# Optimization experiments

Hardware: AMD Instinct MI355X
Metric: run time of the kernel (lower is better)

## Reference

```python
import jax, jax.numpy as jnp
import numpy as np

VOXEL = 64          # voxel_size
MAX_DEPTH = 10.0    # depth_range[1]
SMIN, SMAX = -2.0, 2.0  # spatial_range


def setup_inputs() -> dict:
    key = jax.random.key(0)
    B, H, W = 32, 512, 512
    rgbd = jax.random.uniform(key, (B, 4, H, W), dtype=jnp.float32)
    # scale depth channel to a realistic metric range [0, 8) so that a
    # meaningful fraction of back-projected points falls inside [-2, 2]
    rgbd = rgbd.at[:, 3].multiply(8.0)
    return {"rgbd": rgbd}


def reference(rgbd):
    B, C, H, W = rgbd.shape
    V = VOXEL
    dt = rgbd.dtype

    rgb = jnp.transpose(rgbd[:, :3], (0, 2, 3, 1))   # [B,H,W,3]
    d = rgbd[:, 3]                                   # [B,H,W]

    # intrinsics is None -> default pinhole
    fx = fy = min(H, W) / 2.0
    cx, cy = W / 2.0, H / 2.0

    u = jnp.arange(W, dtype=dt)[None, None, :]       # column index (x)
    v = jnp.arange(H, dtype=dt)[None, :, None]       # row index (y)

    # depth -> pointcloud (per pixel)
    x = (u - cx) * d / fx
    y = (v - cy) * d / fy
    pts = jnp.stack([x, y, d], axis=-1)              # [B,H,W,3]

    depth_valid = (d > 0) & (d < MAX_DEPTH) & jnp.isfinite(d)

    # pointcloud -> voxel coordinates
    coords = jnp.round((pts - SMIN) / (SMAX - SMIN) * (V - 1)).astype(jnp.int32)
    in_range = jnp.all((coords >= 0) & (coords < V), axis=-1)
    mask = depth_valid & in_range                    # [B,H,W]
    coords = jnp.clip(coords, 0, V - 1)

    b_idx = jnp.arange(B, dtype=jnp.int32)[:, None, None]
    lin = ((b_idx * V + coords[..., 0]) * V + coords[..., 1]) * V + coords[..., 2]
    lin = lin.reshape(-1)                            # [B*H*W]
    w = mask.astype(dt).reshape(-1)                  # [B*H*W]

    nseg = B * V * V * V
    count = jax.ops.segment_sum(w, lin, num_segments=nseg)                 # [B*V^3]
    csum = jax.ops.segment_sum(rgb.reshape(-1, 3) * w[:, None], lin,
                               num_segments=nseg)                          # [B*V^3,3]

    occ = (count > 0).astype(dt)                                           # occupancy = 1 where any point lands
    color = jnp.where(count[:, None] > 0,
                      csum / jnp.maximum(count, 1.0)[:, None],
                      jnp.zeros((), dt))                                   # mean color per occupied voxel

    occ = occ.reshape(B, V, V, V)
    color = color.reshape(B, V, V, V, 3).transpose(0, 4, 1, 2, 3)
    return jnp.concatenate([occ[:, None], color], axis=1)  # [B,4,V,V,V]
```

## Files before the change

### kernel.cpp

```cpp
#include <hip/hip_runtime.h>
#include <math.h>


constexpr int V = 64;
constexpr int V3 = V * V * V;
constexpr int Wd = 512, Hd = 512;
constexpr int NPIX = Wd * Hd;
constexpr int NBUCKET = 32 * 64;
constexpr unsigned CAP = 30000;
constexpr float CQ = 32768.0f;

__device__ __forceinline__ bool unproject(int w, int h, float d,
                                          int& ix, int& iy, int& iz) {
    if (!(d > 0.0f) || !(d < 10.0f) || !isfinite(d)) return false;
    const float fx = 256.0f, cx = 256.0f, cy = 256.0f;
    float x = (((float)w - cx) * d) / fx;
    float y = (((float)h - cy) * d) / fx;
    float tx = rintf(((x + 2.0f) * 0.25f) * 63.0f);
    float ty = rintf(((y + 2.0f) * 0.25f) * 63.0f);
    float tz = rintf(((d + 2.0f) * 0.25f) * 63.0f);
    ix = (int)tx; iy = (int)ty; iz = (int)tz;
    return !(ix < 0 || ix >= V || iy < 0 || iy >= V ||
             iz < 0 || iz >= V);
}

__global__ void dtv_cursor_init(unsigned* __restrict__ cursor) {
    int i = blockIdx.x * blockDim.x + threadIdx.x;
    cursor[i] = (unsigned)i * CAP;
}

__global__ void __launch_bounds__(256)
dtv_append2(const float* __restrict__ rgbd,
            unsigned* __restrict__ cursor,
            unsigned long long* __restrict__ entries) {
    int blk = blockIdx.x;
    int b = blk >> 6, chunk = blk & 63, t = threadIdx.x;
    __shared__ unsigned lcnt[64];
    __shared__ unsigned labs[64];
    if (t < 64) lcnt[t] = 0;
    __syncthreads();

    const float* bb = rgbd + (size_t)b * 4 * NPIX;
    const float4* r4 = (const float4*)(bb) + chunk * 1024;
    const float4* g4 = (const float4*)(bb + (size_t)NPIX) + chunk * 1024;
    const float4* b4 = (const float4*)(bb + (size_t)2 * NPIX) + chunk * 1024;
    const float4* d4 = (const float4*)(bb + (size_t)3 * NPIX) + chunk * 1024;
    int pbase = chunk * 4096;

    unsigned meta[16];
#pragma unroll
    for (int i = 0; i < 4; ++i) {
        float4 dv = d4[t + i * 256];
        int p0 = pbase + 4 * (t + i * 256);
#pragma unroll
        for (int j = 0; j < 4; ++j) {
            float d = (j == 0) ? dv.x : (j == 1) ? dv.y : (j == 2) ? dv.z : dv.w;
            int pix = p0 + j;
            int h = pix >> 9, w = pix & (Wd - 1);
            int ix, iy, iz;
            if (unproject(w, h, d, ix, iy, iz)) {
                unsigned off = atomicAdd(&lcnt[ix], 1u);
                meta[i * 4 + j] = ((unsigned)ix << 24) | ((unsigned)iy << 18) |
                                  ((unsigned)iz << 12) | off;
            } else {
                meta[i * 4 + j] = 0xFFFFFFFFu;
            }
        }
    }
    __syncthreads();
    if (t < 64)
        labs[t] = lcnt[t] ? atomicAdd(&cursor[b * 64 + t], lcnt[t]) : 0u;
    __syncthreads();

#pragma unroll
    for (int i = 0; i < 4; ++i) {
        float4 rv = r4[t + i * 256];
        float4 gv = g4[t + i * 256];
        float4 bv = b4[t + i * 256];
#pragma unroll
        for (int j = 0; j < 4; ++j) {
            unsigned m = meta[i * 4 + j];
            if (m == 0xFFFFFFFFu) continue;
            unsigned ix = m >> 24, iy = (m >> 18) & 63u, iz = (m >> 12) & 63u;
            unsigned off = m & 0xFFFu;
            float r  = (j == 0) ? rv.x : (j == 1) ? rv.y : (j == 2) ? rv.z : rv.w;
            float g  = (j == 0) ? gv.x : (j == 1) ? gv.y : (j == 2) ? gv.z : gv.w;
            float bl = (j == 0) ? bv.x : (j == 1) ? bv.y : (j == 2) ? bv.z : bv.w;
            unsigned pos = labs[ix] + off;
            unsigned kk = (unsigned)(b * 64) + ix;
            if (pos >= (kk + 1) * CAP) continue;
            unsigned long long r16 = (unsigned long long)(unsigned)rintf(r  * CQ);
            unsigned long long g16 = (unsigned long long)(unsigned)rintf(g  * CQ);
            unsigned long long b16 = (unsigned long long)(unsigned)rintf(bl * CQ);
            entries[(size_t)pos] = ((unsigned long long)iy << 54) |
                                   ((unsigned long long)iz << 48) |
                                   (r16 << 32) | (g16 << 16) | b16;
        }
    }
}

__global__ void __launch_bounds__(256)
dtv_reduce2(const unsigned long long* __restrict__ entries,
            const unsigned* __restrict__ cursor,
            float* __restrict__ out) {
    int kk = blockIdx.x;
    int b = kk >> 6, ix = kk & 63, t = threadIdx.x;

    __shared__ unsigned long long ldsA[4096];
    __shared__ unsigned long long ldsB[4096];
#pragma unroll
    for (int i = 0; i < 16; ++i) {
        ldsA[t + i * 256] = 0ULL;
        ldsB[t + i * 256] = 0ULL;
    }
    __syncthreads();

    unsigned basew = (unsigned)kk * CAP;
    unsigned cnt = cursor[kk] - basew;
    if (cnt > CAP) cnt = CAP;
    for (unsigned e = t; e < cnt; e += 256) {
        unsigned long long p = entries[(size_t)basew + e];
        unsigned iy = (unsigned)(p >> 54) & 63u;
        unsigned iz = (unsigned)(p >> 48) & 63u;
        unsigned long long r16 = (p >> 32) & 0xFFFFULL;
        unsigned long long gb  = p & 0xFFFFFFFFULL;
        unsigned v = iy * 64u + iz;
        atomicAdd(&ldsA[v], (1ULL << 32) | r16);
        atomicAdd(&ldsB[v], ((gb >> 16) << 32) | (gb & 0xFFFFULL));
    }
    __syncthreads();

    float* p0 = out + (size_t)b * 4 * V3 + (size_t)ix * 4096;
#pragma unroll
    for (int i = 0; i < 16; ++i) {
        int v = t + i * 256;
        unsigned long long A = ldsA[v], Bw = ldsB[v];
        unsigned c = (unsigned)(A >> 32);
        float occ = 0.0f, r = 0.0f, g = 0.0f, bl = 0.0f;
        if (c) {
            float inv = 1.0f / (CQ * (float)c);
            occ = 1.0f;
            r  = (float)(unsigned)(A  & 0xFFFFFFFFULL) * inv;
            g  = (float)(unsigned)(Bw >> 32)            * inv;
            bl = (float)(unsigned)(Bw & 0xFFFFFFFFULL)  * inv;
        }
        p0[v]                  = occ;
        p0[(size_t)V3 + v]     = r;
        p0[(size_t)2 * V3 + v] = g;
        p0[(size_t)3 * V3 + v] = bl;
    }
}

__global__ void dtv_scatter_f32(const float* __restrict__ rgbd,
                                float* __restrict__ acc) {
    int idx = blockIdx.x * blockDim.x + threadIdx.x;
    int b   = idx >> 18;
    int pix = idx & (NPIX - 1);
    int h   = pix >> 9;
    int w   = pix & (Wd - 1);
    const float* base = rgbd + (size_t)b * 4 * NPIX;
    float d = base[(size_t)3 * NPIX + pix];
    int ix, iy, iz;
    if (!unproject(w, h, d, ix, iy, iz)) return;
    float r  = base[pix];
    float g  = base[(size_t)NPIX + pix];
    float bl = base[(size_t)2 * NPIX + pix];
    float* ob = acc + (size_t)b * 4 * V3;
    int vlin = (ix * V + iy) * V + iz;
    atomicAdd(ob + vlin, 1.0f);
    atomicAdd(ob + (size_t)V3 + vlin, r);
    atomicAdd(ob + (size_t)2 * V3 + vlin, g);
    atomicAdd(ob + (size_t)3 * V3 + vlin, bl);
}

__global__ void dtv_finalize_f32(float* __restrict__ out) {
    int idx = blockIdx.x * blockDim.x + threadIdx.x;
    int b    = idx >> 18;
    int vlin = idx & (V3 - 1);
    float* p = out + (size_t)b * 4 * V3;
    float c  = p[vlin];
    float r  = p[(size_t)V3 + vlin];
    float g  = p[(size_t)2 * V3 + vlin];
    float bl = p[(size_t)3 * V3 + vlin];
    bool occ = (c > 0.0f);
    p[vlin]                  = occ ? 1.0f : 0.0f;
    p[(size_t)V3 + vlin]     = occ ? (r / c)  : 0.0f;
    p[(size_t)2 * V3 + vlin] = occ ? (g / c)  : 0.0f;
    p[(size_t)3 * V3 + vlin] = occ ? (bl / c) : 0.0f;
}

extern "C" void kernel_launch(void* const* d_in, const int* in_sizes, int n_in,
                              void* d_out, int out_size, void* d_ws, size_t ws_size,
                              hipStream_t stream) {
    const float* rgbd = (const float*)d_in[0];
    float* out = (float*)d_out;
    const int B = in_sizes[0] / (4 * NPIX);

    size_t need = 8192 + (size_t)NBUCKET * CAP * sizeof(unsigned long long);

    if (B == 32 && ws_size >= need) {
        unsigned* cursor = (unsigned*)d_ws;
        unsigned long long* entries =
            (unsigned long long*)((char*)d_ws + 8192);
        dtv_cursor_init<<<NBUCKET / 256, 256, 0, stream>>>(cursor);
        dtv_append2    <<<2048, 256, 0, stream>>>(rgbd, cursor, entries);
        dtv_reduce2    <<<2048, 256, 0, stream>>>(entries, cursor, out);
    } else {
        hipMemsetAsync(d_out, 0, (size_t)out_size * sizeof(float), stream);
        int total_pix = B * NPIX;
        int total_vox = B * V3;
        dtv_scatter_f32 <<<(total_pix + 255) / 256, 256, 0, stream>>>(rgbd, out);
        dtv_finalize_f32<<<(total_vox + 255) / 256, 256, 0, stream>>>(out);
    }
}
```

Baseline: 286.7 us.

## Stage bucketed entries in LDS and write them out coalesced per bucket

The append kernel now halves the pixels per block (2048) and doubles the block count. Each block does a wave-level prefix scan over its 64 per-ix bucket counts, sorts its entries into shared memory by bucket, and then writes them to global memory in contiguous runs. Before, each thread scattered its 8-byte writes straight to global. The aim is to turn scattered global stores into mostly coalesced ones. The cost is an extra LDS pass, another barrier and about 20KB of shared memory per block, plus twice as many global cursor atomics.

```diff
diff --git a/kernel.cpp b/kernel.cpp
--- a/kernel.cpp
+++ b/kernel.cpp
@@ -9,6 +9,8 @@
 constexpr int NBUCKET = 32 * 64;
 constexpr unsigned CAP = 30000;
 constexpr float CQ = 32768.0f;
+constexpr int PPB = 2048;
+constexpr int CHUNKS = NPIX / PPB;
 
 __device__ __forceinline__ bool unproject(int w, int h, float d,
                                           int& ix, int& iy, int& iz) {
@@ -30,26 +32,31 @@
 }
 
 __global__ void __launch_bounds__(256)
-dtv_append2(const float* __restrict__ rgbd,
+dtv_append3(const float* __restrict__ rgbd,
             unsigned* __restrict__ cursor,
             unsigned long long* __restrict__ entries) {
     int blk = blockIdx.x;
-    int b = blk >> 6, chunk = blk & 63, t = threadIdx.x;
+    int b = blk >> 7, chunk = blk & (CHUNKS - 1), t = threadIdx.x;
+
     __shared__ unsigned lcnt[64];
+    __shared__ unsigned lpre[64];
     __shared__ unsigned labs[64];
+    __shared__ unsigned long long stage[PPB];
+    __shared__ unsigned short bkt[PPB];
+
     if (t < 64) lcnt[t] = 0;
     __syncthreads();
 
     const float* bb = rgbd + (size_t)b * 4 * NPIX;
-    const float4* r4 = (const float4*)(bb) + chunk * 1024;
-    const float4* g4 = (const float4*)(bb + (size_t)NPIX) + chunk * 1024;
-    const float4* b4 = (const float4*)(bb + (size_t)2 * NPIX) + chunk * 1024;
-    const float4* d4 = (const float4*)(bb + (size_t)3 * NPIX) + chunk * 1024;
-    int pbase = chunk * 4096;
-
-    unsigned meta[16];
-#pragma unroll
-    for (int i = 0; i < 4; ++i) {
+    const float4* r4 = (const float4*)(bb) + chunk * (PPB / 4);
+    const float4* g4 = (const float4*)(bb + (size_t)NPIX) + chunk * (PPB / 4);
+    const float4* b4 = (const float4*)(bb + (size_t)2 * NPIX) + chunk * (PPB / 4);
+    const float4* d4 = (const float4*)(bb + (size_t)3 * NPIX) + chunk * (PPB / 4);
+    int pbase = chunk * PPB;
+
+    unsigned meta[8];
+#pragma unroll
+    for (int i = 0; i < 2; ++i) {
         float4 dv = d4[t + i * 256];
         int p0 = pbase + 4 * (t + i * 256);
 #pragma unroll
@@ -68,12 +75,22 @@
         }
     }
     __syncthreads();
-    if (t < 64)
-        labs[t] = lcnt[t] ? atomicAdd(&cursor[b * 64 + t], lcnt[t]) : 0u;
-    __syncthreads();
-
-#pragma unroll
-    for (int i = 0; i < 4; ++i) {
+
+    if (t < 64) {
+        unsigned c = lcnt[t];
+        unsigned s = c;
+#pragma unroll
+        for (int off = 1; off < 64; off <<= 1) {
+            unsigned v = __shfl_up(s, off, 64);
+            if (t >= off) s += v;
+        }
+        lpre[t] = s - c;
+        labs[t] = c ? atomicAdd(&cursor[b * 64 + t], c) : 0u;
+    }
+    __syncthreads();
+
+#pragma unroll
+    for (int i = 0; i < 2; ++i) {
         float4 rv = r4[t + i * 256];
         float4 gv = g4[t + i * 256];
         float4 bv = b4[t + i * 256];
@@ -86,16 +103,25 @@
             float r  = (j == 0) ? rv.x : (j == 1) ? rv.y : (j == 2) ? rv.z : rv.w;
             float g  = (j == 0) ? gv.x : (j == 1) ? gv.y : (j == 2) ? gv.z : gv.w;
             float bl = (j == 0) ? bv.x : (j == 1) ? bv.y : (j == 2) ? bv.z : bv.w;
-            unsigned pos = labs[ix] + off;
-            unsigned kk = (unsigned)(b * 64) + ix;
-            if (pos >= (kk + 1) * CAP) continue;
             unsigned long long r16 = (unsigned long long)(unsigned)rintf(r  * CQ);
             unsigned long long g16 = (unsigned long long)(unsigned)rintf(g  * CQ);
             unsigned long long b16 = (unsigned long long)(unsigned)rintf(bl * CQ);
-            entries[(size_t)pos] = ((unsigned long long)iy << 54) |
-                                   ((unsigned long long)iz << 48) |
-                                   (r16 << 32) | (g16 << 16) | b16;
-        }
+            unsigned slot = lpre[ix] + off;
+            stage[slot] = ((unsigned long long)iy << 54) |
+                          ((unsigned long long)iz << 48) |
+                          (r16 << 32) | (g16 << 16) | b16;
+            bkt[slot] = (unsigned short)ix;
+        }
+    }
+    __syncthreads();
+
+    unsigned total = lpre[63] + lcnt[63];
+    for (unsigned e = t; e < total; e += 256) {
+        unsigned ix = bkt[e];
+        unsigned pos = labs[ix] + (e - lpre[ix]);
+        unsigned kk = (unsigned)(b * 64) + ix;
+        if (pos < (kk + 1) * CAP)
+            entries[(size_t)pos] = stage[e];
     }
 }
 
@@ -203,8 +229,8 @@
         unsigned long long* entries =
             (unsigned long long*)((char*)d_ws + 8192);
         dtv_cursor_init<<<NBUCKET / 256, 256, 0, stream>>>(cursor);
-        dtv_append2    <<<2048, 256, 0, stream>>>(rgbd, cursor, entries);
-        dtv_reduce2    <<<2048, 256, 0, stream>>>(entries, cursor, out);
+        dtv_append3    <<<B * CHUNKS, 256, 0, stream>>>(rgbd, cursor, entries);
+        dtv_reduce2    <<<NBUCKET, 256, 0, stream>>>(entries, cursor, out);
     } else {
         hipMemsetAsync(d_out, 0, (size_t)out_size * sizeof(float), stream);
         int total_pix = B * NPIX;
```

Result: faster. 259.2 us (-9.6%).
